# Performance work log

Measured on AMD Instinct MI355X. Metric: run time of the kernel, lower is better.

Reference implementation:

```python
import jax, jax.numpy as jnp
import numpy as np

ROW = 48   # num_row_points
COL = 48   # num_column_points
K = 21     # kernel_size


def _grid_sample_translate(ker, tx, ty):
    """Bilinear grid_sample (zeros padding, align_corners=True) for a pure
    per-image translation grid. ker: [N, h, w]; tx, ty: [N] normalized shifts.
    Matches F.affine_grid(identity + translation) + F.grid_sample."""
    N, h, w = ker.shape
    dt = ker.dtype
    # source pixel coords: px = x_out + tx*(w-1)/2 (align_corners=True)
    px = jnp.arange(w, dtype=dt)[None, :] + tx[:, None] * (w - 1) / 2  # [N, w]
    py = jnp.arange(h, dtype=dt)[None, :] + ty[:, None] * (h - 1) / 2  # [N, h]

    x0 = jnp.floor(px); fx = px - x0
    def gat_w(i):
        m = ((i >= 0) & (i <= w - 1)).astype(dt)
        ic = jnp.clip(i, 0, w - 1).astype(jnp.int32)
        v = jnp.take_along_axis(ker, jnp.broadcast_to(ic[:, None, :], ker.shape), axis=2)
        return v * m[:, None, :]
    gx = gat_w(x0) * (1 - fx)[:, None, :] + gat_w(x0 + 1) * fx[:, None, :]

    y0 = jnp.floor(py); fy = py - y0
    def gat_h(i):
        m = ((i >= 0) & (i <= h - 1)).astype(dt)
        ic = jnp.clip(i, 0, h - 1).astype(jnp.int32)
        v = jnp.take_along_axis(gx, jnp.broadcast_to(ic[:, :, None], gx.shape), axis=1)
        return v * m[:, :, None]
    return gat_h(y0) * (1 - fy)[:, :, None] + gat_h(y0 + 1) * fy[:, :, None]


def setup_inputs() -> dict:
    key = jax.random.key(0)
    k1, k2, k3 = jax.random.split(key, 3)
    N = ROW * COL
    inp = jax.random.normal(k1, (4, 64, 192, 192), dtype=jnp.float32)
    # torch.rand init; floor at 0.05 to avoid a degenerate zero sigma draw
    sigma_x = jax.random.uniform(k2, (N,), dtype=jnp.float32, minval=0.05, maxval=1.0)
    sigma_y = jax.random.uniform(k3, (N,), dtype=jnp.float32, minval=0.05, maxval=1.0)
    opacity = jnp.ones((N, 1), dtype=jnp.float32)
    return {"inp": inp, "sigma_x": sigma_x, "sigma_y": sigma_y, "opacity": opacity}


def reference(inp, sigma_x, sigma_y, opacity):
    B, C, H, W = inp.shape
    nbr, nbc = H // ROW, W // COL
    L = nbr * nbc
    N = ROW * COL

    # Unfold into non-overlapping ROWxCOL patches -> [B*L, C, ROW, COL]
    patches = (inp.reshape(B, C, nbr, ROW, nbc, COL)
                  .transpose(0, 2, 4, 1, 3, 5)
                  .reshape(B * L, C, ROW, COL))
    colors = patches.reshape(B * L, C, N).transpose(0, 2, 1)  # [BL, N, C]

    # meshgrid point coords: index k = i*COL + j, x=j (col), y=i (row)
    ii, jj = jnp.meshgrid(jnp.arange(ROW), jnp.arange(COL), indexing="ij")
    i = ii.reshape(-1).astype(inp.dtype)
    j = jj.reshape(-1).astype(inp.dtype)
    # coords_norm = (0.5 - [x/ROW, y/COL]) * 2  (note: x divided by height, as in source)
    tx = 1.0 - 2.0 * j / ROW
    ty = 1.0 - 2.0 * i / COL

    # per-point axis-aligned Gaussian kernel on [-5, 5]^2
    ax = jnp.linspace(-5.0, 5.0, K).astype(inp.dtype)
    xx2 = (ax ** 2)[None, :, None]  # x varies along first kernel dim
    yy2 = (ax ** 2)[None, None, :]
    sx2 = (sigma_x ** 2)[:, None, None]
    sy2 = (sigma_y ** 2)[:, None, None]
    z = -0.5 * (xx2 / sx2 + yy2 / sy2)                      # [N, K, K]
    kernel = jnp.exp(z) / (2.0 * jnp.pi * jnp.sqrt(sx2 * sy2))
    kernel = kernel / kernel.max(axis=(1, 2), keepdims=True)

    pad_h, pad_w = ROW - K, COL - K
    kp = jnp.pad(kernel, ((0, 0),
                          (pad_h // 2, pad_h // 2 + pad_h % 2),
                          (pad_w // 2, pad_w // 2 + pad_w % 2)))
    kt = _grid_sample_translate(kp, tx, ty)                  # [N, ROW, COL]

    weighted = colors * opacity[None, :, :]                  # [BL, N, C]
    out = jnp.einsum("bpc,phw->bchw", weighted, kt)          # splat-accumulate
    out = jnp.clip(out, 0.0, 1.0)

    # Fold back to [B, C, H, W]
    out = (out.reshape(B, nbr, nbc, C, ROW, COL)
              .transpose(0, 3, 1, 4, 2, 5)
              .reshape(B, C, H, W))
    return out
```

## Files before the change

kernel.cpp:

```cpp
#include <hip/hip_runtime.h>


#define NPTS 2304
#define KD   2304
#define HH   192

typedef _Float16 f16;
typedef _Float16 f16x8 __attribute__((ext_vector_type(8)));
typedef float f32x4 __attribute__((ext_vector_type(4)));

__device__ __forceinline__ void gload16(const f16* g, f16* l) {
    __builtin_amdgcn_global_load_lds((const __attribute__((address_space(1))) void*)g,
                                     (__attribute__((address_space(3))) void*)l,
                                     16, 0, 0);
}

__device__ __forceinline__ float gtap(float t, float inv2s) {
    float ax = 0.5f * t - 11.5f;
    float g = expf(-ax * ax * inv2s);
    return (t >= 12.5f && t <= 33.5f) ? g : 0.0f;
}

__global__ void build_kykx(const float* __restrict__ sx, const float* __restrict__ sy,
                           const float* __restrict__ op,
                           float* __restrict__ KY_T, float* __restrict__ KX_T) {
    int flat = blockIdx.x * 256 + threadIdx.x;
    if (flat >= 48 * NPTS) return;
    int pos = flat / NPTS;
    int p   = flat - pos * NPTS;
    int i = p / 48;
    int j = p - i * 48;
    float sxv = sx[p], syv = sy[p], opv = op[p];
    float invx = 0.5f / (sxv * sxv);
    float invy = 0.5f / (syv * syv);

    float py = (float)pos + 23.5f - (47.0f / 48.0f) * (float)i;
    float y0 = floorf(py), fy = py - y0;
    KY_T[flat] = opv * (gtap(y0, invx) * (1.0f - fy) + gtap(y0 + 1.0f, invx) * fy);

    float px = (float)pos + 23.5f - (47.0f / 48.0f) * (float)j;
    float x0 = floorf(px), fx = px - x0;
    KX_T[flat] = gtap(x0, invy) * (1.0f - fx) + gtap(x0 + 1.0f, invy) * fx;
}

__global__ void build_kt(const float* __restrict__ KY_T, const float* __restrict__ KX_T,
                         f16* __restrict__ Kt) {
    int idx = blockIdx.x * 256 + threadIdx.x;
    int hw = idx / 288;
    int p0 = (idx - hw * 288) * 8;
    int y = hw / 48, x = hw - y * 48;
    const float4* ky = (const float4*)(KY_T + (size_t)y * NPTS + p0);
    const float4* kx = (const float4*)(KX_T + (size_t)x * NPTS + p0);
    float4 a0 = ky[0], a1 = ky[1];
    float4 b0 = kx[0], b1 = kx[1];
    f16x8 r;
    r[0] = (f16)(a0.x * b0.x); r[1] = (f16)(a0.y * b0.y);
    r[2] = (f16)(a0.z * b0.z); r[3] = (f16)(a0.w * b0.w);
    r[4] = (f16)(a1.x * b1.x); r[5] = (f16)(a1.y * b1.y);
    r[6] = (f16)(a1.z * b1.z); r[7] = (f16)(a1.w * b1.w);
    *(f16x8*)(Kt + (size_t)hw * NPTS + p0) = r;
}

__global__ void pack_A(const float* __restrict__ inp, f16* __restrict__ A) {
    int idx = blockIdx.x * 256 + threadIdx.x;
    int m = idx / 288;
    int p0 = (idx - m * 288) * 8;
    int i = p0 / 48, j = p0 - i * 48;
    int bl = m >> 6, c = m & 63;
    int b = bl >> 4, pr = (bl >> 2) & 3, pc = bl & 3;
    const float* src = inp + ((size_t)(b * 64 + c) * HH + pr * 48 + i) * HH + pc * 48 + j;
    float4 a0 = *(const float4*)src;
    float4 a1 = *(const float4*)(src + 4);
    f16x8 r;
    r[0] = (f16)a0.x; r[1] = (f16)a0.y; r[2] = (f16)a0.z; r[3] = (f16)a0.w;
    r[4] = (f16)a1.x; r[5] = (f16)a1.y; r[6] = (f16)a1.z; r[7] = (f16)a1.w;
    *(f16x8*)(A + (size_t)m * KD + p0) = r;
}

__global__ __launch_bounds__(256) void gemm_splat(const f16* __restrict__ A,
                                                  const f16* __restrict__ Bt,
                                                  float* __restrict__ out) {
    __shared__ __attribute__((aligned(16))) f16 As[128 * 32];
    __shared__ __attribute__((aligned(16))) f16 Bs[128 * 32];

    int tid  = threadIdx.x;
    int lane = tid & 63;
    int w    = tid >> 6;
    int wr   = w >> 1, wc = w & 1;
    int bx   = blockIdx.x;
    int m0   = (bx / 18) * 128;
    int n0   = (bx % 18) * 128;

    int y_min = n0 / 48;
    int y_max = (n0 + 127) / 48;
    int i_lo = max(0,  (int)floorf((y_min - 10.5f) * (48.0f / 47.0f)));
    int i_hi = min(47, (int)ceilf ((y_max + 11.5f) * (48.0f / 47.0f)));
    int k_lo = (i_lo * 48) & ~31;
    int k_hi = min(KD, ((i_hi + 1) * 48 + 31) & ~31);

    int srow = lane >> 2;
    int sko  = (lane & 3) * 8;

    const int lrow = lane & 15;
    const int lk8  = (lane >> 4) * 8;

    f32x4 acc[4][4] = {};

    for (int k0 = k_lo; k0 < k_hi; k0 += 32) {
        #pragma unroll
        for (int c = 0; c < 2; ++c) {
            int r   = w + c * 4;
            int row = r * 16 + srow;
            gload16(&A [(size_t)(m0 + row) * KD + k0 + sko], &As[r * 512]);
            gload16(&Bt[(size_t)(n0 + row) * KD + k0 + sko], &Bs[r * 512]);
        }
        __syncthreads();

        f16x8 af[4], bf[4];
        #pragma unroll
        for (int mi = 0; mi < 4; ++mi)
            af[mi] = *(const f16x8*)&As[(wr * 64 + mi * 16 + lrow) * 32 + lk8];
        #pragma unroll
        for (int ni = 0; ni < 4; ++ni)
            bf[ni] = *(const f16x8*)&Bs[(wc * 64 + ni * 16 + lrow) * 32 + lk8];

        #pragma unroll
        for (int mi = 0; mi < 4; ++mi)
            #pragma unroll
            for (int ni = 0; ni < 4; ++ni)
                acc[mi][ni] = __builtin_amdgcn_mfma_f32_16x16x32_f16(af[mi], bf[ni], acc[mi][ni], 0, 0, 0);
        __syncthreads();
    }

    #pragma unroll
    for (int mi = 0; mi < 4; ++mi) {
        #pragma unroll
        for (int r = 0; r < 4; ++r) {
            int m  = m0 + wr * 64 + mi * 16 + (lane >> 4) * 4 + r;
            int bl = m >> 6, c = m & 63;
            int b  = bl >> 4, pr = (bl >> 2) & 3, pc = bl & 3;
            float* orow = out + ((size_t)(b * 64 + c) * HH + pr * 48) * HH + pc * 48;
            #pragma unroll
            for (int ni = 0; ni < 4; ++ni) {
                int n = n0 + wc * 64 + ni * 16 + (lane & 15);
                int y = n / 48, x = n - y * 48;
                float v = acc[mi][ni][r];
                v = fminf(fmaxf(v, 0.0f), 1.0f);
                orow[y * HH + x] = v;
            }
        }
    }
}

extern "C" void kernel_launch(void* const* d_in, const int* in_sizes, int n_in,
                              void* d_out, int out_size, void* d_ws, size_t ws_size,
                              hipStream_t stream) {
    const float* inp = (const float*)d_in[0];
    const float* sx  = (const float*)d_in[1];
    const float* sy  = (const float*)d_in[2];
    const float* op  = (const float*)d_in[3];
    float* out = (float*)d_out;

    char* ws = (char*)d_ws;
    float* KY_T = (float*)ws;
    float* KX_T = (float*)(ws + 442368);
    f16*   Kt   = (f16*)(ws + 884736);
    f16*   Ap   = (f16*)(ws + 884736 + 10616832);

    build_kykx<<<dim3(432),  dim3(256), 0, stream>>>(sx, sy, op, KY_T, KX_T);
    build_kt  <<<dim3(2592), dim3(256), 0, stream>>>(KY_T, KX_T, Kt);
    pack_A    <<<dim3(4608), dim3(256), 0, stream>>>(inp, Ap);
    gemm_splat<<<dim3(576),  dim3(256), 0, stream>>>(Ap, Kt, out);
}
```

Before: 146.4 us.

## Double-buffer GEMM LDS tiles, swizzle layout, and halve N tile width

```diff
diff --git a/kernel.cpp b/kernel.cpp
--- a/kernel.cpp
+++ b/kernel.cpp
@@ -80,57 +80,66 @@
 __global__ __launch_bounds__(256) void gemm_splat(const f16* __restrict__ A,
                                                   const f16* __restrict__ Bt,
                                                   float* __restrict__ out) {
-    __shared__ __attribute__((aligned(16))) f16 As[128 * 32];
-    __shared__ __attribute__((aligned(16))) f16 Bs[128 * 32];
+    __shared__ __attribute__((aligned(16))) f16 As[2 * 4096];
+    __shared__ __attribute__((aligned(16))) f16 Bs[2 * 2048];
 
     int tid  = threadIdx.x;
     int lane = tid & 63;
     int w    = tid >> 6;
     int wr   = w >> 1, wc = w & 1;
     int bx   = blockIdx.x;
-    int m0   = (bx / 18) * 128;
-    int n0   = (bx % 18) * 128;
+    int m0   = (bx / 36) * 128;
+    int n0   = (bx % 36) * 64;
 
     int y_min = n0 / 48;
-    int y_max = (n0 + 127) / 48;
+    int y_max = (n0 + 63) / 48;
     int i_lo = max(0,  (int)floorf((y_min - 10.5f) * (48.0f / 47.0f)));
     int i_hi = min(47, (int)ceilf ((y_max + 11.5f) * (48.0f / 47.0f)));
     int k_lo = (i_lo * 48) & ~31;
     int k_hi = min(KD, ((i_hi + 1) * 48 + 31) & ~31);
+    int nt   = (k_hi - k_lo) >> 5;
 
     int srow = lane >> 2;
-    int sko  = (lane & 3) * 8;
+    int sk   = (((lane & 3) ^ ((lane >> 3) & 3)) << 3);
+    const f16* Abase = A  + (size_t)(m0 + w * 32 + srow) * KD + sk;
+    const f16* Bbase = Bt + (size_t)(n0 + w * 16 + srow) * KD + sk;
 
-    const int lrow = lane & 15;
-    const int lk8  = (lane >> 4) * 8;
+    int lrow = lane & 15;
+    int koe  = (((lane >> 4) ^ ((lane >> 1) & 3)) << 3);
 
-    f32x4 acc[4][4] = {};
+    f32x4 acc[4][2] = {};
 
-    for (int k0 = k_lo; k0 < k_hi; k0 += 32) {
-        #pragma unroll
-        for (int c = 0; c < 2; ++c) {
-            int r   = w + c * 4;
-            int row = r * 16 + srow;
-            gload16(&A [(size_t)(m0 + row) * KD + k0 + sko], &As[r * 512]);
-            gload16(&Bt[(size_t)(n0 + row) * KD + k0 + sko], &Bs[r * 512]);
-        }
-        __syncthreads();
+    #define STAGE(buf, k0)                                                      \
+        do {                                                                    \
+            gload16(Abase + (k0),           &As[(buf) * 4096 + (w * 2 + 0) * 512]); \
+            gload16(Abase + 16 * KD + (k0), &As[(buf) * 4096 + (w * 2 + 1) * 512]); \
+            gload16(Bbase + (k0),           &Bs[(buf) * 2048 + w * 512]);           \
+        } while (0)
 
-        f16x8 af[4], bf[4];
+    STAGE(0, k_lo);
+    __syncthreads();
+
+    for (int t = 0; t < nt; ++t) {
+        int cur = t & 1;
+        if (t + 1 < nt) STAGE(cur ^ 1, k_lo + ((t + 1) << 5));
+
+        f16x8 af[4], bf[2];
         #pragma unroll
         for (int mi = 0; mi < 4; ++mi)
-            af[mi] = *(const f16x8*)&As[(wr * 64 + mi * 16 + lrow) * 32 + lk8];
+            af[mi] = *(const f16x8*)&As[cur * 4096 + (wr * 64 + mi * 16 + lrow) * 32 + koe];
         #pragma unroll
-        for (int ni = 0; ni < 4; ++ni)
-            bf[ni] = *(const f16x8*)&Bs[(wc * 64 + ni * 16 + lrow) * 32 + lk8];
+        for (int ni = 0; ni < 2; ++ni)
+            bf[ni] = *(const f16x8*)&Bs[cur * 2048 + (wc * 32 + ni * 16 + lrow) * 32 + koe];
 
         #pragma unroll
         for (int mi = 0; mi < 4; ++mi)
             #pragma unroll
-            for (int ni = 0; ni < 4; ++ni)
+            for (int ni = 0; ni < 2; ++ni)
                 acc[mi][ni] = __builtin_amdgcn_mfma_f32_16x16x32_f16(af[mi], bf[ni], acc[mi][ni], 0, 0, 0);
+
         __syncthreads();
     }
+    #undef STAGE
 
     #pragma unroll
     for (int mi = 0; mi < 4; ++mi) {
@@ -141,8 +150,8 @@
             int b  = bl >> 4, pr = (bl >> 2) & 3, pc = bl & 3;
             float* orow = out + ((size_t)(b * 64 + c) * HH + pr * 48) * HH + pc * 48;
             #pragma unroll
-            for (int ni = 0; ni < 4; ++ni) {
-                int n = n0 + wc * 64 + ni * 16 + (lane & 15);
+            for (int ni = 0; ni < 2; ++ni) {
+                int n = n0 + wc * 32 + ni * 16 + (lane & 15);
                 int y = n / 48, x = n - y * 48;
                 float v = acc[mi][ni][r];
                 v = fminf(fmaxf(v, 0.0f), 1.0f);
@@ -170,5 +179,5 @@
     build_kykx<<<dim3(432),  dim3(256), 0, stream>>>(sx, sy, op, KY_T, KX_T);
     build_kt  <<<dim3(2592), dim3(256), 0, stream>>>(KY_T, KX_T, Kt);
     pack_A    <<<dim3(4608), dim3(256), 0, stream>>>(inp, Ap);
-    gemm_splat<<<dim3(576),  dim3(256), 0, stream>>>(Ap, Kt, out);
+    gemm_splat<<<dim3(1152), dim3(256), 0, stream>>>(Ap, Kt, out);
 }
```

Result: slower. 155.3 us (+6.1%).

## Fuse input packing into GEMM with double-buffered swizzled LDS and banded Kt build

Applied to the files above, without the earlier changes.

```diff
diff --git a/kernel.cpp b/kernel.cpp
--- a/kernel.cpp
+++ b/kernel.cpp
@@ -6,6 +6,7 @@
 #define HH   192
 
 typedef _Float16 f16;
+typedef _Float16 f16x4 __attribute__((ext_vector_type(4)));
 typedef _Float16 f16x8 __attribute__((ext_vector_type(8)));
 typedef float f32x4 __attribute__((ext_vector_type(4)));
 
@@ -15,13 +16,23 @@
                                      16, 0, 0);
 }
 
+__device__ __forceinline__ void kwindow(int tt, int& k_lo, int& k_hi) {
+    int n0 = tt * 128;
+    int y_min = n0 / 48;
+    int y_max = (n0 + 127) / 48;
+    int i_lo = max(0,  (int)floorf((y_min - 10.5f) * (48.0f / 47.0f)));
+    int i_hi = min(47, (int)ceilf ((y_max + 11.5f) * (48.0f / 47.0f)));
+    k_lo = (i_lo * 48) & ~31;
+    k_hi = min(KD, ((i_hi + 1) * 48 + 31) & ~31);
+}
+
 __device__ __forceinline__ float gtap(float t, float inv2s) {
     float ax = 0.5f * t - 11.5f;
     float g = expf(-ax * ax * inv2s);
     return (t >= 12.5f && t <= 33.5f) ? g : 0.0f;
 }
 
-__global__ void build_kykx(const float* __restrict__ sx, const float* __restrict__ sy,
+__global__ void build_tabs(const float* __restrict__ sx, const float* __restrict__ sy,
                            const float* __restrict__ op,
                            float* __restrict__ KY_T, float* __restrict__ KX_T) {
     int flat = blockIdx.x * 256 + threadIdx.x;
@@ -46,8 +57,12 @@
 __global__ void build_kt(const float* __restrict__ KY_T, const float* __restrict__ KX_T,
                          f16* __restrict__ Kt) {
     int idx = blockIdx.x * 256 + threadIdx.x;
-    int hw = idx / 288;
-    int p0 = (idx - hw * 288) * 8;
+    int hw = idx / 176;
+    int ci = idx - hw * 176;
+    int k_lo, k_hi;
+    kwindow(hw >> 7, k_lo, k_hi);
+    int p0 = k_lo + ci * 8;
+    if (p0 >= k_hi) return;
     int y = hw / 48, x = hw - y * 48;
     const float4* ky = (const float4*)(KY_T + (size_t)y * NPTS + p0);
     const float4* kx = (const float4*)(KX_T + (size_t)x * NPTS + p0);
@@ -61,85 +76,125 @@
     *(f16x8*)(Kt + (size_t)hw * NPTS + p0) = r;
 }
 
-__global__ void pack_A(const float* __restrict__ inp, f16* __restrict__ A) {
-    int idx = blockIdx.x * 256 + threadIdx.x;
-    int m = idx / 288;
-    int p0 = (idx - m * 288) * 8;
-    int i = p0 / 48, j = p0 - i * 48;
-    int bl = m >> 6, c = m & 63;
-    int b = bl >> 4, pr = (bl >> 2) & 3, pc = bl & 3;
-    const float* src = inp + ((size_t)(b * 64 + c) * HH + pr * 48 + i) * HH + pc * 48 + j;
-    float4 a0 = *(const float4*)src;
-    float4 a1 = *(const float4*)(src + 4);
-    f16x8 r;
-    r[0] = (f16)a0.x; r[1] = (f16)a0.y; r[2] = (f16)a0.z; r[3] = (f16)a0.w;
-    r[4] = (f16)a1.x; r[5] = (f16)a1.y; r[6] = (f16)a1.z; r[7] = (f16)a1.w;
-    *(f16x8*)(A + (size_t)m * KD + p0) = r;
-}
-
-__global__ __launch_bounds__(256) void gemm_splat(const f16* __restrict__ A,
+__global__ __launch_bounds__(256) void gemm_splat(const float* __restrict__ inp,
                                                   const f16* __restrict__ Bt,
                                                   float* __restrict__ out) {
-    __shared__ __attribute__((aligned(16))) f16 As[128 * 32];
-    __shared__ __attribute__((aligned(16))) f16 Bs[128 * 32];
+    __shared__ __attribute__((aligned(16))) f16 As[2 * 4096];
+    __shared__ __attribute__((aligned(16))) f16 Bs[2 * 4096];
 
     int tid  = threadIdx.x;
     int lane = tid & 63;
     int w    = tid >> 6;
     int wr   = w >> 1, wc = w & 1;
     int bx   = blockIdx.x;
-    int m0   = (bx / 18) * 128;
-    int n0   = (bx % 18) * 128;
-
-    int y_min = n0 / 48;
-    int y_max = (n0 + 127) / 48;
-    int i_lo = max(0,  (int)floorf((y_min - 10.5f) * (48.0f / 47.0f)));
-    int i_hi = min(47, (int)ceilf ((y_max + 11.5f) * (48.0f / 47.0f)));
-    int k_lo = (i_lo * 48) & ~31;
-    int k_hi = min(KD, ((i_hi + 1) * 48 + 31) & ~31);
+    int wg   = (bx & 7) * 72 + (bx >> 3);
+    int m0   = (wg / 18) * 128;
+    int tt   = wg % 18;
+    int n0   = tt * 128;
+
+    int k_lo, k_hi;
+    kwindow(tt, k_lo, k_hi);
+    int nt = (k_hi - k_lo) >> 5;
 
     int srow = lane >> 2;
-    int sko  = (lane & 3) * 8;
-
-    const int lrow = lane & 15;
-    const int lk8  = (lane >> 4) * 8;
+    int sk   = (((lane & 3) ^ ((lane >> 3) & 3)) << 3);
+    const f16* Bbase = Bt + (size_t)(n0 + w * 32 + srow) * KD + sk + k_lo;
+
+    int bl = (m0 >> 6) + (w >> 1);
+    int b = bl >> 4, pr = (bl >> 2) & 3, pc = bl & 3;
+    const float* ibase = inp + ((size_t)(b * 64) * HH + pr * 48) * HH + pc * 48;
+    int c0 = (w & 1) * 32 + (lane >> 3);
+    const float* pA0 = ibase + (size_t)c0 * (HH * HH);
+    int kl = k_lo + (lane & 7) * 4;
+    int ii = kl / 48;
+    int jj = kl - ii * 48;
+    int off = ii * HH + jj;
+    int aw = (w * 32 + (lane >> 3)) * 32 + ((((lane >> 1) & 3) ^ (lane >> 4)) << 3) + (lane & 1) * 4;
+
+    int lrow = lane & 15;
+    int koe  = (((lane >> 4) ^ ((lane >> 1) & 3)) << 3);
 
     f32x4 acc[4][4] = {};
-
-    for (int k0 = k_lo; k0 < k_hi; k0 += 32) {
-        #pragma unroll
-        for (int c = 0; c < 2; ++c) {
-            int r   = w + c * 4;
-            int row = r * 16 + srow;
-            gload16(&A [(size_t)(m0 + row) * KD + k0 + sko], &As[r * 512]);
-            gload16(&Bt[(size_t)(n0 + row) * KD + k0 + sko], &Bs[r * 512]);
+    float4 av0, av1, av2, av3;
+
+    #define ALOAD()                                             \
+        do {                                                    \
+            av0 = *(const float4*)(pA0 + off);                  \
+            av1 = *(const float4*)(pA0 +  8 * HH * HH + off);   \
+            av2 = *(const float4*)(pA0 + 16 * HH * HH + off);   \
+            av3 = *(const float4*)(pA0 + 24 * HH * HH + off);   \
+        } while (0)
+    #define AWRITE(slot)                                                          \
+        do {                                                                      \
+            f16* as_ = &As[(slot) * 4096 + aw];                                   \
+            f16x4 h;                                                              \
+            h[0]=(f16)av0.x; h[1]=(f16)av0.y; h[2]=(f16)av0.z; h[3]=(f16)av0.w;   \
+            *(f16x4*)(as_      ) = h;                                             \
+            h[0]=(f16)av1.x; h[1]=(f16)av1.y; h[2]=(f16)av1.z; h[3]=(f16)av1.w;   \
+            *(f16x4*)(as_ + 256) = h;                                             \
+            h[0]=(f16)av2.x; h[1]=(f16)av2.y; h[2]=(f16)av2.z; h[3]=(f16)av2.w;   \
+            *(f16x4*)(as_ + 512) = h;                                             \
+            h[0]=(f16)av3.x; h[1]=(f16)av3.y; h[2]=(f16)av3.z; h[3]=(f16)av3.w;   \
+            *(f16x4*)(as_ + 768) = h;                                             \
+        } while (0)
+    #define AADV()                                              \
+        do {                                                    \
+            int jn = jj + 32;                                   \
+            int ov = (jn >= 48);                                \
+            off += ov ? (HH - 48 + 32) : 32;                    \
+            jj  = ov ? jn - 48 : jn;                            \
+        } while (0)
+
+    ALOAD();
+    gload16(Bbase,           &Bs[w * 1024]);
+    gload16(Bbase + 16 * KD, &Bs[w * 1024 + 512]);
+    AWRITE(0);
+    AADV();
+    __syncthreads();
+
+    for (int t = 0; t < nt; ++t) {
+        int cur = t & 1;
+        bool more = (t + 1 < nt);
+        if (more) {
+            ALOAD();
+            gload16(Bbase + ((t + 1) << 5),           &Bs[(cur ^ 1) * 4096 + w * 1024]);
+            gload16(Bbase + 16 * KD + ((t + 1) << 5), &Bs[(cur ^ 1) * 4096 + w * 1024 + 512]);
         }
-        __syncthreads();
 
         f16x8 af[4], bf[4];
         #pragma unroll
         for (int mi = 0; mi < 4; ++mi)
-            af[mi] = *(const f16x8*)&As[(wr * 64 + mi * 16 + lrow) * 32 + lk8];
+            af[mi] = *(const f16x8*)&As[cur * 4096 + (wr * 64 + mi * 16 + lrow) * 32 + koe];
         #pragma unroll
         for (int ni = 0; ni < 4; ++ni)
-            bf[ni] = *(const f16x8*)&Bs[(wc * 64 + ni * 16 + lrow) * 32 + lk8];
-
+            bf[ni] = *(const f16x8*)&Bs[cur * 4096 + (wc * 64 + ni * 16 + lrow) * 32 + koe];
+
+        __builtin_amdgcn_s_setprio(1);
         #pragma unroll
         for (int mi = 0; mi < 4; ++mi)
             #pragma unroll
             for (int ni = 0; ni < 4; ++ni)
                 acc[mi][ni] = __builtin_amdgcn_mfma_f32_16x16x32_f16(af[mi], bf[ni], acc[mi][ni], 0, 0, 0);
+        __builtin_amdgcn_s_setprio(0);
+
+        if (more) {
+            AWRITE(cur ^ 1);
+            AADV();
+        }
         __syncthreads();
     }
+    #undef ALOAD
+    #undef AWRITE
+    #undef AADV
 
     #pragma unroll
     for (int mi = 0; mi < 4; ++mi) {
         #pragma unroll
         for (int r = 0; r < 4; ++r) {
             int m  = m0 + wr * 64 + mi * 16 + (lane >> 4) * 4 + r;
-            int bl = m >> 6, c = m & 63;
-            int b  = bl >> 4, pr = (bl >> 2) & 3, pc = bl & 3;
-            float* orow = out + ((size_t)(b * 64 + c) * HH + pr * 48) * HH + pc * 48;
+            int blm = m >> 6, c = m & 63;
+            int bb  = blm >> 4, prm = (blm >> 2) & 3, pcm = blm & 3;
+            float* orow = out + ((size_t)(bb * 64 + c) * HH + prm * 48) * HH + pcm * 48;
             #pragma unroll
             for (int ni = 0; ni < 4; ++ni) {
                 int n = n0 + wc * 64 + ni * 16 + (lane & 15);
@@ -165,10 +220,8 @@
     float* KY_T = (float*)ws;
     float* KX_T = (float*)(ws + 442368);
     f16*   Kt   = (f16*)(ws + 884736);
-    f16*   Ap   = (f16*)(ws + 884736 + 10616832);
-
-    build_kykx<<<dim3(432),  dim3(256), 0, stream>>>(sx, sy, op, KY_T, KX_T);
-    build_kt  <<<dim3(2592), dim3(256), 0, stream>>>(KY_T, KX_T, Kt);
-    pack_A    <<<dim3(4608), dim3(256), 0, stream>>>(inp, Ap);
-    gemm_splat<<<dim3(576),  dim3(256), 0, stream>>>(Ap, Kt, out);
-}
+
+    build_tabs<<<dim3(432),  dim3(256), 0, stream>>>(sx, sy, op, KY_T, KX_T);
+    build_kt  <<<dim3(1584), dim3(256), 0, stream>>>(KY_T, KX_T, Kt);
+    gemm_splat<<<dim3(576),  dim3(256), 0, stream>>>(inp, Kt, out);
+}
```

Measured after the change: 140.1 us. 4.3% less time.
